# Optimization experiments

Measured on AMD Instinct MI355X. Metric: run time of the kernel, lower is better.

The kernel has to match this reference:

```python
import jax, jax.numpy as jnp
import numpy as np
import math

B, H, L = 8, 512, 4096
N2 = 32  # d_state // 2


def setup_inputs() -> dict:
    key = jax.random.key(0)
    ks = jax.random.split(key, 8)
    u = jax.random.normal(ks[0], (B, H, L), dtype=jnp.float32)
    C = jax.random.normal(ks[1], (H, N2, 2), dtype=jnp.float32)  # view_as_real of cfloat C
    # log_dt ~ Uniform[log(dt_min), log(dt_max)], dt_min=1e-3, dt_max=0.1
    log_dt = jax.random.uniform(ks[2], (H,), dtype=jnp.float32,
                                minval=math.log(0.001), maxval=math.log(0.1))
    log_A_real = jnp.log(0.5 * jnp.ones((H, N2), dtype=jnp.float32))
    A_imag = math.pi * jnp.broadcast_to(jnp.arange(N2, dtype=jnp.float32), (H, N2))
    D = jax.random.normal(ks[3], (H,), dtype=jnp.float32)
    # pointwise Conv1d(H, 2H, kernel_size=1): weight (2H, H), bias (2H)
    fan = 1.0 / math.sqrt(H)
    W = jax.random.uniform(ks[4], (2 * H, H), dtype=jnp.float32, minval=-fan, maxval=fan)
    b = jax.random.uniform(ks[5], (2 * H,), dtype=jnp.float32, minval=-fan, maxval=fan)
    return {"u": u, "C": C, "log_dt": log_dt, "log_A_real": log_A_real,
            "A_imag": A_imag, "D": D, "W": W, "b": b}


def reference(u, C, log_dt, log_A_real, A_imag, D, W, b):
    Lb = u.shape[-1]
    # --- S4DKernel: kernel k of shape (H, L) ---
    dt = jnp.exp(log_dt)                                  # (H,)
    Cc = C[..., 0] + 1j * C[..., 1]                       # (H, N2) complex
    A = -jnp.exp(log_A_real) + 1j * A_imag                # (H, N2)
    dtA = A * dt[:, None]                                 # (H, N2)
    # Vandermonde: exp(dtA * l) for l in [0, L)
    K = jnp.exp(dtA[:, :, None] * jnp.arange(Lb, dtype=jnp.float32))  # (H, N2, L)
    Cmod = Cc * (jnp.exp(dtA) - 1.0) / A                  # (H, N2)
    k = 2.0 * jnp.einsum('hn,hnl->hl', Cmod, K).real      # (H, L)
    # --- FFT convolution (length 2L, causal) ---
    n = 2 * Lb
    k_f = jnp.fft.rfft(k, n=n)                            # (H, L+1)
    u_f = jnp.fft.rfft(u, n=n)                            # (B, H, L+1)
    y = jnp.fft.irfft(u_f * k_f, n=n)[..., :Lb]           # (B, H, L)
    # skip connection
    y = y + u * D[:, None]
    # activation (torch nn.GELU default = exact erf form)
    y = jax.nn.gelu(y, approximate=False)
    # pointwise conv (H -> 2H) + GLU over channel dim
    y = jnp.einsum('oh,bhl->bol', W, y) + b[None, :, None]  # (B, 2H, L)
    a, g = jnp.split(y, 2, axis=1)
    return a * jax.nn.sigmoid(g)                          # (B, H, L)
```

## Files before the change

### kernel.cpp

```cpp
#include <hip/hip_runtime.h>
#include <hip/hip_bf16.h>

constexpr int Bn = 8, Hn = 512, Ln = 4096, N2n = 32;

typedef _Float16 f16;
typedef __attribute__((ext_vector_type(8))) _Float16 f16x8;
typedef __attribute__((ext_vector_type(4))) _Float16 f16x4;
typedef __attribute__((ext_vector_type(2))) _Float16 f16x2;
typedef __attribute__((ext_vector_type(4))) float f32x4;

typedef void __attribute__((address_space(1))) gvoid;
typedef void __attribute__((address_space(3))) lvoid;

__global__ __launch_bounds__(64) void k_mats1(
    const float* __restrict__ C, const float* __restrict__ log_dt,
    const float* __restrict__ logA, const float* __restrict__ Aim,
    f16* __restrict__ Vg, f16* __restrict__ A3g, float2* __restrict__ w64g) {
  __shared__ f16 VT[64 * 64];
  __shared__ f16 QT[64 * 64];
  __shared__ float kp[64][33];
  __shared__ float ks[64];
  const int h = blockIdx.x, tid = threadIdx.x, n = tid & 31;

  if (tid < 32) {
    const int idx = h * N2n + n;
    float dt = expf(log_dt[h]);
    float Ar = -expf(logA[idx]);
    float Ai = Aim[idx];
    float dr = Ar * dt, di = Ai * dt;
    float er = expf(dr);
    float wr = er * cosf(di), wi = er * sinf(di);
    float den = Ar * Ar + Ai * Ai;
    float e1r = wr - 1.0f, e1i = wi;
    float tr = (e1r * Ar + e1i * Ai) / den;
    float ti = (e1i * Ar - e1r * Ai) / den;
    float Cr = C[idx * 2 + 0], Ci = C[idx * 2 + 1];
    float c2r = 2.0f * (Cr * tr - Ci * ti);
    float c2i = 2.0f * (Cr * ti + Ci * tr);

    float wpr = 1.f, wpi = 0.f;
    for (int p = 0; p <= 64; ++p) {
      float cwr = c2r * wpr - c2i * wpi;
      float cwi = c2r * wpi + c2i * wpr;
      if (p < 64) {
        const int j = 63 - p, ch = j >> 3, jo = j & 7;
        const int s0 = 2 * n, s1 = 2 * n + 1;
        VT[s0 * 64 + ((ch ^ (s0 & 7)) * 8) + jo] = (f16)wpr;
        VT[s1 * 64 + ((ch ^ (s1 & 7)) * 8) + jo] = (f16)wpi;
        kp[p][n] = cwr;
      }
      if (p >= 1) {
        const int t = p - 1, c0 = 2 * n;
        const int ch = (c0 >> 3) ^ (t & 7);
        QT[t * 64 + ch * 8 + (c0 & 7)]     = (f16)cwr;
        QT[t * 64 + ch * 8 + (c0 & 7) + 1] = (f16)(-cwi);
      }
      if (p == 64) w64g[h * 32 + n] = make_float2(wpr, wpi);
      float nr = wpr * wr - wpi * wi;
      float ni = wpr * wi + wpi * wr;
      wpr = nr; wpi = ni;
    }
  }
  __syncthreads();
  float s = 0.f;
#pragma unroll
  for (int m = 0; m < 32; ++m) s += kp[tid][m];
  ks[tid] = s;
  __syncthreads();
  const int t = tid;
#pragma unroll
  for (int c = 0; c < 8; ++c) {
    f16x8 row;
#pragma unroll
    for (int jo = 0; jo < 8; ++jo) {
      int j = c * 8 + jo;
      row[jo] = (j <= t) ? (f16)ks[t - j] : (f16)0.f;
    }
    *(f16x8*)&A3g[(size_t)h * 8192 + t * 128 + ((c ^ (t & 7)) * 8)] = row;
  }
#pragma unroll
  for (int c = 0; c < 8; ++c)
    *(f16x8*)&Vg[(size_t)h * 4096 + tid * 64 + c * 8] = *(f16x8*)&VT[tid * 64 + c * 8];
#pragma unroll
  for (int c = 0; c < 8; ++c)
    *(f16x8*)&A3g[(size_t)h * 8192 + tid * 128 + 64 + c * 8] = *(f16x8*)&QT[tid * 64 + c * 8];
}

__global__ void conv_w(const float* __restrict__ W, f16* __restrict__ Wh) {
  int i = blockIdx.x * 256 + threadIdx.x;
  if (i < 2 * Hn * Hn) Wh[i] = (f16)W[i];
}

__global__ __launch_bounds__(256, 4) void s4d_mid(
    const float* __restrict__ u, const f16* __restrict__ Vg,
    const f16* __restrict__ A3g, const float2* __restrict__ w64g,
    const float* __restrict__ Dv, f16* __restrict__ yg) {
  __shared__ f16 MATS[8192];
  __shared__ f16 U[4096];
  __shared__ f16 LE[4096];
  __shared__ float2 Pbuf[4][32];
  const int tid = threadIdx.x, wid = tid >> 6, lane = tid & 63;
  const int h = ((blockIdx.x >> 6) << 3) | (blockIdx.x & 7);
  const int b = (blockIdx.x >> 3) & 7;
  const float Dh = Dv[h];

#pragma unroll
  for (int q = 0; q < 2; ++q)
    __builtin_amdgcn_global_load_lds((const gvoid*)(Vg + (size_t)h * 4096 + (q * 256 + tid) * 8),
                                     (lvoid*)&MATS[(q * 256 + wid * 64) * 8], 16, 0, 0);
#pragma unroll
  for (int i = 0; i < 4; ++i) {
    int e = (i * 256 + tid) * 4;
    float4 uv = *(const float4*)(u + ((size_t)(b * Hn + h)) * Ln + e);
    int col = e >> 6, j = e & 63;
    f16x4 hv = {(f16)uv.x, (f16)uv.y, (f16)uv.z, (f16)uv.w};
    *(f16x4*)&U[col * 64 + ((j >> 3) ^ (col & 7)) * 8 + (j & 7)] = hv;
  }
  asm volatile("s_waitcnt vmcnt(0)" ::: "memory");
  __syncthreads();

  const int col = wid * 16 + (lane & 15);
  f32x4 acc[4];
#pragma unroll
  for (int i = 0; i < 4; ++i) acc[i] = (f32x4){0.f, 0.f, 0.f, 0.f};
#pragma unroll
  for (int ks = 0; ks < 2; ++ks) {
    const int kc = ks * 4 + (lane >> 4);
    f16x8 bv = *(const f16x8*)&U[col * 64 + ((kc ^ (col & 7)) * 8)];
#pragma unroll
    for (int mf = 0; mf < 4; ++mf) {
      int row = mf * 16 + (lane & 15);
      f16x8 a = *(const f16x8*)&MATS[row * 64 + ((kc ^ (row & 7)) * 8)];
      acc[mf] = __builtin_amdgcn_mfma_f32_16x16x32_f16(a, bv, acc[mf], 0, 0, 0);
    }
  }
  __syncthreads();

#pragma unroll
  for (int q = 0; q < 4; ++q)
    __builtin_amdgcn_global_load_lds((const gvoid*)(A3g + (size_t)h * 8192 + (q * 256 + tid) * 8),
                                     (lvoid*)&MATS[(q * 256 + wid * 64) * 8], 16, 0, 0);

#pragma unroll
  for (int mf = 0; mf < 4; ++mf) {
    int st0 = mf * 16 + (lane >> 4) * 4;
    f16x4 o = {(f16)acc[mf][0], (f16)acc[mf][1], (f16)acc[mf][2], (f16)acc[mf][3]};
    *(f16x4*)&LE[col * 64 + (((st0 >> 3) ^ (col & 7)) << 3) + (st0 & 7)] = o;
  }
  __syncthreads();

  {
    const int n = lane & 31, q = wid;
    const float2 wT = w64g[h * 32 + n];
    float qr = wT.x, qi = wT.y;
#pragma unroll
    for (int s = 0; s < 4; ++s) {
      float nr = qr * qr - qi * qi;
      float ni = 2.f * qr * qi;
      qr = nr; qi = ni;
    }
    f16x2 Lb[16];
    float er = 0.f, ei = 0.f;
    if (lane < 32) {
#pragma unroll
      for (int k = 0; k < 16; ++k) {
        int blk = q * 16 + k;
        int fi = blk * 64 + (((n >> 2) ^ (blk & 7)) << 3) + ((n & 3) << 1);
        Lb[k] = *(const f16x2*)&LE[fi];
      }
#pragma unroll
      for (int k = 0; k < 16; ++k) {
        float nr = fmaf(wT.x, er, fmaf(-wT.y, ei, (float)Lb[k][0]));
        float ni = fmaf(wT.y, er, fmaf(wT.x, ei, (float)Lb[k][1]));
        er = nr; ei = ni;
      }
      Pbuf[q][n] = make_float2(er, ei);
    }
    __syncthreads();
    if (lane < 32) {
      float orr = 0.f, oii = 0.f;
      for (int p = 0; p < q; ++p) {
        float2 Pp = Pbuf[p][n];
        float nr = fmaf(qr, orr, fmaf(-qi, oii, Pp.x));
        float ni = fmaf(qi, orr, fmaf(qr, oii, Pp.y));
        orr = nr; oii = ni;
      }
      er = orr; ei = oii;
#pragma unroll
      for (int k = 0; k < 16; ++k) {
        int blk = q * 16 + k;
        int fi = blk * 64 + (((n >> 2) ^ (blk & 7)) << 3) + ((n & 3) << 1);
        *(f16x2*)&LE[fi] = (f16x2){(f16)er, (f16)ei};
        float nr = fmaf(wT.x, er, fmaf(-wT.y, ei, (float)Lb[k][0]));
        float ni = fmaf(wT.y, er, fmaf(wT.x, ei, (float)Lb[k][1]));
        er = nr; ei = ni;
      }
    }
  }
  asm volatile("s_waitcnt vmcnt(0)" ::: "memory");
  __syncthreads();

  f32x4 acc4[4];
#pragma unroll
  for (int i = 0; i < 4; ++i) acc4[i] = (f32x4){0.f, 0.f, 0.f, 0.f};
#pragma unroll
  for (int ks = 0; ks < 4; ++ks) {
    const int kc = ks * 4 + (lane >> 4);
    f16x8 bf;
    if (ks < 2) bf = *(const f16x8*)&U[col * 64 + ((kc ^ (col & 7)) << 3)];
    else        bf = *(const f16x8*)&LE[col * 64 + (((kc - 8) ^ (col & 7)) << 3)];
#pragma unroll
    for (int mf = 0; mf < 4; ++mf) {
      int row = mf * 16 + (lane & 15);
      f16x8 af = *(const f16x8*)&MATS[row * 128 + ((kc ^ (row & 7)) << 3)];
      acc4[mf] = __builtin_amdgcn_mfma_f32_16x16x32_f16(af, bf, acc4[mf], 0, 0, 0);
    }
  }
  const int t0 = (lane >> 4) * 4;
#pragma unroll
  for (int mf = 0; mf < 4; ++mf) {
    const int tb = mf * 16 + t0;
    f16x4 uq = *(const f16x4*)&U[col * 64 + (((tb >> 3) ^ (col & 7)) << 3) + (tb & 7)];
    f16x4 o;
#pragma unroll
    for (int r = 0; r < 4; ++r) {
      float v = acc4[mf][r] + Dh * (float)uq[r];
      float g2 = v * fmaf(0.0713548163f, v * v, 1.5957691216f);
      o[r] = (f16)(v * __builtin_amdgcn_rcpf(1.0f + __expf(-g2)));
    }
    *(f16x4*)&yg[((size_t)(b * Hn + h)) * Ln + col * 64 + tb] = o;
  }
}

__global__ __launch_bounds__(256) void k_transpose(
    const f16* __restrict__ yg, f16* __restrict__ gyT) {
  __shared__ float T[64][65];
  const int bid = blockIdx.x, tid = threadIdx.x;
  const int b = bid >> 9, hg = (bid >> 6) & 7, lg = bid & 63;
  const int h0 = hg * 64, l0 = lg * 64;
  const int hi = tid >> 2, lc = (tid & 3) * 16;
  const f16* src = yg + ((size_t)(b * Hn + h0 + hi)) * Ln + l0 + lc;
  f16x8 v0 = *(const f16x8*)src;
  f16x8 v1 = *(const f16x8*)(src + 8);
#pragma unroll
  for (int e = 0; e < 8; ++e) T[lc + e][hi] = (float)v0[e];
#pragma unroll
  for (int e = 0; e < 8; ++e) T[lc + 8 + e][hi] = (float)v1[e];
  __syncthreads();
  const int li = tid >> 2, hc = (tid & 3) * 16;
  f16x8 o0, o1;
#pragma unroll
  for (int e = 0; e < 8; ++e) o0[e] = (f16)T[li][hc + e];
#pragma unroll
  for (int e = 0; e < 8; ++e) o1[e] = (f16)T[li][hc + 8 + e];
  f16* dst = gyT + ((size_t)b * Ln + l0 + li) * Hn + h0 + hc;
  *(f16x8*)dst = o0;
  *(f16x8*)(dst + 8) = o1;
}

__global__ __launch_bounds__(256, 2) void s4d_gemm(
    const f16* __restrict__ Wh, const f16* __restrict__ gyT,
    const float* __restrict__ bias, float* __restrict__ out) {
  __shared__ f16 As[2][128][64];
  __shared__ f16 Bs[128][64];
  const int tid = threadIdx.x;
  const int wid = tid >> 6, lane = tid & 63;
  const int ntg = blockIdx.x & 255;
  const int mt = blockIdx.x >> 8;
  const int b = ntg >> 5;
  const int l0 = (ntg & 31) * 128;
  const int m0 = mt * 128;
  const int wm = wid >> 1, wn = wid & 1;

  f32x4 acc[2][4][4];
#pragma unroll
  for (int a = 0; a < 2; ++a)
#pragma unroll
    for (int i = 0; i < 4; ++i)
#pragma unroll
      for (int j = 0; j < 4; ++j) acc[a][i][j] = (f32x4){0.f, 0.f, 0.f, 0.f};

  const int srow = lane >> 3;
  const int sks = ((lane & 7) ^ srow) * 8;

  for (int kt = 0; kt < 8; ++kt) {
    const int k0 = kt * 64;
#pragma unroll
    for (int q = 0; q < 4; ++q) {
      const int r8 = wid * 32 + q * 8;
      const f16* srcA = Wh + ((size_t)(m0 + r8 + srow) * 512 + k0 + sks);
      __builtin_amdgcn_global_load_lds((const gvoid*)srcA, (lvoid*)&As[0][r8][0], 16, 0, 0);
      const f16* srcG = Wh + ((size_t)(Hn + m0 + r8 + srow) * 512 + k0 + sks);
      __builtin_amdgcn_global_load_lds((const gvoid*)srcG, (lvoid*)&As[1][r8][0], 16, 0, 0);
      const f16* srcB = gyT + (((size_t)b * Ln + l0 + r8 + srow) * Hn + k0 + sks);
      __builtin_amdgcn_global_load_lds((const gvoid*)srcB, (lvoid*)&Bs[r8][0], 16, 0, 0);
    }
    asm volatile("s_waitcnt vmcnt(0)" ::: "memory");
    __syncthreads();
#pragma unroll
    for (int kk = 0; kk < 2; ++kk) {
      const int kc = kk * 4 + (lane >> 4);
      f16x8 af0[4], af1[4], bfv[4];
#pragma unroll
      for (int mf = 0; mf < 4; ++mf) {
        const int row = wm * 64 + mf * 16 + (lane & 15);
        af0[mf] = *(const f16x8*)&As[0][row][(kc ^ (row & 7)) * 8];
        af1[mf] = *(const f16x8*)&As[1][row][(kc ^ (row & 7)) * 8];
      }
#pragma unroll
      for (int nf = 0; nf < 4; ++nf) {
        const int col = wn * 64 + nf * 16 + (lane & 15);
        bfv[nf] = *(const f16x8*)&Bs[col][(kc ^ (col & 7)) * 8];
      }
#pragma unroll
      for (int mf = 0; mf < 4; ++mf)
#pragma unroll
        for (int nf = 0; nf < 4; ++nf) {
          acc[0][mf][nf] = __builtin_amdgcn_mfma_f32_16x16x32_f16(af0[mf], bfv[nf], acc[0][mf][nf], 0, 0, 0);
          acc[1][mf][nf] = __builtin_amdgcn_mfma_f32_16x16x32_f16(af1[mf], bfv[nf], acc[1][mf][nf], 0, 0, 0);
        }
    }
    __syncthreads();
  }

  const int col = lane & 15, r0 = (lane >> 4) * 4;
#pragma unroll
  for (int mf = 0; mf < 4; ++mf) {
    const int hbase = m0 + wm * 64 + mf * 16 + r0;
#pragma unroll
    for (int nf = 0; nf < 4; ++nf) {
      const int l = l0 + wn * 64 + nf * 16 + col;
      f32x4 va = acc[0][mf][nf], vg = acc[1][mf][nf];
#pragma unroll
      for (int r = 0; r < 4; ++r) {
        const int hh = hbase + r;
        float av = va[r] + bias[hh];
        float gv = vg[r] + bias[Hn + hh];
        float sg = __builtin_amdgcn_rcpf(1.0f + __expf(-gv));
        out[((size_t)b * Hn + hh) * Ln + l] = av * sg;
      }
    }
  }
}

extern "C" void kernel_launch(void* const* d_in, const int* in_sizes, int n_in,
                              void* d_out, int out_size, void* d_ws, size_t ws_size,
                              hipStream_t stream) {
  (void)in_sizes; (void)n_in; (void)out_size; (void)ws_size;
  const float* u     = (const float*)d_in[0];
  const float* C     = (const float*)d_in[1];
  const float* logdt = (const float*)d_in[2];
  const float* logA  = (const float*)d_in[3];
  const float* Aim   = (const float*)d_in[4];
  const float* Dv    = (const float*)d_in[5];
  const float* W     = (const float*)d_in[6];
  const float* bias  = (const float*)d_in[7];
  float* out = (float*)d_out;

  char* ws = (char*)d_ws;
  f16*    gyT  = (f16*)ws;
  f16*    Vg   = (f16*)(ws + (size_t)(32 << 20));
  f16*    A3g  = (f16*)(ws + (size_t)(36 << 20));
  float2* w64g = (float2*)(ws + (size_t)(44 << 20));
  f16*    Wh   = (f16*)(ws + (size_t)(45 << 20));
  f16*    yg   = (f16*)d_out;

  hipLaunchKernelGGL(k_mats1, dim3(Hn), dim3(64), 0, stream, C, logdt, logA, Aim, Vg, A3g, w64g);
  hipLaunchKernelGGL(conv_w, dim3(2048), dim3(256), 0, stream, W, Wh);
  hipLaunchKernelGGL(s4d_mid, dim3(Hn * Bn), dim3(256), 0, stream, u, Vg, A3g, w64g, Dv, yg);
  hipLaunchKernelGGL(k_transpose, dim3(Bn * 8 * 64), dim3(256), 0, stream, yg, gyT);
  hipLaunchKernelGGL(s4d_gemm, dim3(4 * 256), dim3(256), 0, stream, Wh, gyT, bias, out);
}
```

Before: 98.12 us.

## Enlarge GEMM tiles, double-buffer LDS loads, split gate/value waves

The final GLU GEMM goes from 256-thread blocks with 128x128 tiles to 512-thread blocks covering 256 output rows (128 value plus 128 gate) by 256 columns. The k-loop now double-buffers LDS so the next k-slice loads while the current one computes. Gate waves compute the sigmoid and hand it to value waves through LDS as fp16, and bias is cached in shared memory. The aim is more operand reuse, fewer blocks and overlap of loads with MFMA, at the cost of higher LDS use and register pressure, plus fp16 rounding of the gate value.

New measurement: 103.1 us. +5.1%, slower.

```diff
diff --git a/kernel.cpp b/kernel.cpp
--- a/kernel.cpp
+++ b/kernel.cpp
@@ -258,89 +258,124 @@
   *(f16x8*)(dst + 8) = o1;
 }
 
-__global__ __launch_bounds__(256, 2) void s4d_gemm(
+__global__ __launch_bounds__(512, 2) void s4d_gemm(
     const f16* __restrict__ Wh, const f16* __restrict__ gyT,
     const float* __restrict__ bias, float* __restrict__ out) {
-  __shared__ f16 As[2][128][64];
-  __shared__ f16 Bs[128][64];
+  __shared__ f16 Asd[2][256 * 64];
+  __shared__ f16 Bsd[2][256 * 64];
+  __shared__ float biasS[256];
   const int tid = threadIdx.x;
   const int wid = tid >> 6, lane = tid & 63;
-  const int ntg = blockIdx.x & 255;
-  const int mt = blockIdx.x >> 8;
-  const int b = ntg >> 5;
-  const int l0 = (ntg & 31) * 128;
+  const int nt = blockIdx.x & 127;
+  const int mt = blockIdx.x >> 7;
+  const int b = nt >> 4;
+  const int l0 = (nt & 15) * 256;
   const int m0 = mt * 128;
-  const int wm = wid >> 1, wn = wid & 1;
-
-  f32x4 acc[2][4][4];
-#pragma unroll
-  for (int a = 0; a < 2; ++a)
-#pragma unroll
-    for (int i = 0; i < 4; ++i)
-#pragma unroll
-      for (int j = 0; j < 4; ++j) acc[a][i][j] = (f32x4){0.f, 0.f, 0.f, 0.f};
-
-  const int srow = lane >> 3;
-  const int sks = ((lane & 7) ^ srow) * 8;
+  const int isG = wid >> 2;
+  const int w4 = wid & 3;
+
+  if (tid < 128) biasS[tid] = bias[m0 + tid];
+  else if (tid < 256) biasS[tid] = bias[Hn + m0 + (tid - 128)];
+
+  const int srow8 = lane >> 3;
+  const int sp = lane & 7;
+
+#define STAGE(BUF, KT)                                                                   \
+  {                                                                                      \
+    const int k0 = (KT) * 64;                                                            \
+    _Pragma("unroll")                                                                    \
+    for (int q = 0; q < 4; ++q) {                                                        \
+      const int r = q * 64 + wid * 8 + srow8;                                \
+      const int wr = (r < 128) ? (m0 + r) : (Hn + m0 + r - 128);                         \
+      const f16* srcA = Wh + ((size_t)wr * 512 + k0 + ((sp ^ (r & 7)) * 8));             \
+      __builtin_amdgcn_global_load_lds((const gvoid*)srcA,                               \
+          (lvoid*)&Asd[BUF][(q * 64 + wid * 8) * 64], 16, 0, 0);                         \
+    }                                                                                    \
+    _Pragma("unroll")                                                                    \
+    for (int q = 0; q < 4; ++q) {                                                        \
+      const int r = q * 64 + wid * 8 + srow8;                          \
+      const f16* srcB = gyT + (((size_t)b * Ln + l0 + r) * Hn + k0 + ((sp ^ (r & 7)) * 8)); \
+      __builtin_amdgcn_global_load_lds((const gvoid*)srcB,                               \
+          (lvoid*)&Bsd[BUF][(q * 64 + wid * 8) * 64], 16, 0, 0);                         \
+    }                                                                                    \
+  }
+
+  f32x4 acc[8][4];
+#pragma unroll
+  for (int i = 0; i < 8; ++i)
+#pragma unroll
+    for (int j = 0; j < 4; ++j) acc[i][j] = (f32x4){0.f, 0.f, 0.f, 0.f};
+
+  STAGE(0, 0);
+  asm volatile("s_waitcnt vmcnt(0)" ::: "memory");
+  __syncthreads();
 
   for (int kt = 0; kt < 8; ++kt) {
-    const int k0 = kt * 64;
-#pragma unroll
-    for (int q = 0; q < 4; ++q) {
-      const int r8 = wid * 32 + q * 8;
-      const f16* srcA = Wh + ((size_t)(m0 + r8 + srow) * 512 + k0 + sks);
-      __builtin_amdgcn_global_load_lds((const gvoid*)srcA, (lvoid*)&As[0][r8][0], 16, 0, 0);
-      const f16* srcG = Wh + ((size_t)(Hn + m0 + r8 + srow) * 512 + k0 + sks);
-      __builtin_amdgcn_global_load_lds((const gvoid*)srcG, (lvoid*)&As[1][r8][0], 16, 0, 0);
-      const f16* srcB = gyT + (((size_t)b * Ln + l0 + r8 + srow) * Hn + k0 + sks);
-      __builtin_amdgcn_global_load_lds((const gvoid*)srcB, (lvoid*)&Bs[r8][0], 16, 0, 0);
+    const int cur = kt & 1;
+    if (kt < 7) STAGE(cur ^ 1, kt + 1);
+#pragma unroll
+    for (int kk = 0; kk < 2; ++kk) {
+      const int kc = kk * 4 + (lane >> 4);
+      f16x8 bf[4];
+#pragma unroll
+      for (int nf = 0; nf < 4; ++nf) {
+        const int cl = w4 * 64 + nf * 16 + (lane & 15);
+        bf[nf] = *(const f16x8*)&Bsd[cur][cl * 64 + ((kc ^ (cl & 7)) * 8)];
+      }
+#pragma unroll
+      for (int mf = 0; mf < 8; ++mf) {
+        const int ra = isG * 128 + mf * 16 + (lane & 15);
+        f16x8 af = *(const f16x8*)&Asd[cur][ra * 64 + ((kc ^ (ra & 7)) * 8)];
+#pragma unroll
+        for (int nf = 0; nf < 4; ++nf)
+          acc[mf][nf] = __builtin_amdgcn_mfma_f32_16x16x32_f16(af, bf[nf], acc[mf][nf], 0, 0, 0);
+      }
     }
     asm volatile("s_waitcnt vmcnt(0)" ::: "memory");
     __syncthreads();
-#pragma unroll
-    for (int kk = 0; kk < 2; ++kk) {
-      const int kc = kk * 4 + (lane >> 4);
-      f16x8 af0[4], af1[4], bfv[4];
-#pragma unroll
-      for (int mf = 0; mf < 4; ++mf) {
-        const int row = wm * 64 + mf * 16 + (lane & 15);
-        af0[mf] = *(const f16x8*)&As[0][row][(kc ^ (row & 7)) * 8];
-        af1[mf] = *(const f16x8*)&As[1][row][(kc ^ (row & 7)) * 8];
-      }
-#pragma unroll
-      for (int nf = 0; nf < 4; ++nf) {
-        const int col = wn * 64 + nf * 16 + (lane & 15);
-        bfv[nf] = *(const f16x8*)&Bs[col][(kc ^ (col & 7)) * 8];
-      }
-#pragma unroll
-      for (int mf = 0; mf < 4; ++mf)
-#pragma unroll
-        for (int nf = 0; nf < 4; ++nf) {
-          acc[0][mf][nf] = __builtin_amdgcn_mfma_f32_16x16x32_f16(af0[mf], bfv[nf], acc[0][mf][nf], 0, 0, 0);
-          acc[1][mf][nf] = __builtin_amdgcn_mfma_f32_16x16x32_f16(af1[mf], bfv[nf], acc[1][mf][nf], 0, 0, 0);
+  }
+
+  f16* SIG = &Asd[0][0];
+  const int slot = (w4 * 64 + lane) * 128;
+  if (isG) {
+#pragma unroll
+    for (int mf = 0; mf < 8; ++mf) {
+#pragma unroll
+      for (int np = 0; np < 2; ++np) {
+        f16x8 c;
+#pragma unroll
+        for (int e = 0; e < 8; ++e) {
+          const int nf = np * 2 + (e >> 2), r = e & 3;
+          const int rowh = mf * 16 + (lane >> 4) * 4 + r;
+          float gv = acc[mf][nf][r] + biasS[128 + rowh];
+          c[e] = (f16)__builtin_amdgcn_rcpf(1.0f + __expf(-gv));
         }
-    }
-    __syncthreads();
-  }
-
-  const int col = lane & 15, r0 = (lane >> 4) * 4;
-#pragma unroll
-  for (int mf = 0; mf < 4; ++mf) {
-    const int hbase = m0 + wm * 64 + mf * 16 + r0;
-#pragma unroll
-    for (int nf = 0; nf < 4; ++nf) {
-      const int l = l0 + wn * 64 + nf * 16 + col;
-      f32x4 va = acc[0][mf][nf], vg = acc[1][mf][nf];
-#pragma unroll
-      for (int r = 0; r < 4; ++r) {
-        const int hh = hbase + r;
-        float av = va[r] + bias[hh];
-        float gv = vg[r] + bias[Hn + hh];
-        float sg = __builtin_amdgcn_rcpf(1.0f + __expf(-gv));
-        out[((size_t)b * Hn + hh) * Ln + l] = av * sg;
-      }
-    }
-  }
+        const int cid = mf * 2 + np;
+        *(f16x8*)&SIG[slot + ((cid ^ (lane & 15)) * 8)] = c;
+      }
+    }
+  }
+  __syncthreads();
+  if (!isG) {
+#pragma unroll
+    for (int mf = 0; mf < 8; ++mf) {
+#pragma unroll
+      for (int np = 0; np < 2; ++np) {
+        const int cid = mf * 2 + np;
+        f16x8 sg = *(const f16x8*)&SIG[slot + ((cid ^ (lane & 15)) * 8)];
+#pragma unroll
+        for (int e = 0; e < 8; ++e) {
+          const int nf = np * 2 + (e >> 2), r = e & 3;
+          const int rowh = mf * 16 + (lane >> 4) * 4 + r;
+          const int hh = m0 + rowh;
+          const int l = l0 + w4 * 64 + nf * 16 + (lane & 15);
+          float av = acc[mf][nf][r] + biasS[rowh];
+          out[((size_t)b * Hn + hh) * Ln + l] = av * (float)sg[e];
+        }
+      }
+    }
+  }
+#undef STAGE
 }
 
 extern "C" void kernel_launch(void* const* d_in, const int* in_sizes, int n_in,
@@ -369,5 +404,5 @@
   hipLaunchKernelGGL(conv_w, dim3(2048), dim3(256), 0, stream, W, Wh);
   hipLaunchKernelGGL(s4d_mid, dim3(Hn * Bn), dim3(256), 0, stream, u, Vg, A3g, w64g, Dv, yg);
   hipLaunchKernelGGL(k_transpose, dim3(Bn * 8 * 64), dim3(256), 0, stream, yg, gyT);
-  hipLaunchKernelGGL(s4d_gemm, dim3(4 * 256), dim3(256), 0, stream, Wh, gyT, bias, out);
-}
+  hipLaunchKernelGGL(s4d_gemm, dim3(512), dim3(512), 0, stream, Wh, gyT, bias, out);
+}
```

## Restructure GLU GEMM with double-buffered K=32 stages and split gate/value warps

Applied to the files above, without the earlier changes.

Rewrites the final pointwise-conv GEMM to use 64-row M tiles, which doubles the grid. Warps are split so half compute the value half of the output and half compute the gate half, with sigmoid results exchanged through shared memory. K is staged in 32-wide chunks with double-buffered async global-to-LDS loads, so the next tile loads while MFMAs run. Bias is cached in LDS and occupancy is raised to 3 blocks per SM, aiming for better latency hiding and fewer registers. The cost is an extra LDS round trip for the gate values stored as f16, which loses some precision, plus extra barriers.

New measurement: 107.7 us. 9.8% more time.

```diff
diff --git a/kernel.cpp b/kernel.cpp
--- a/kernel.cpp
+++ b/kernel.cpp
@@ -258,89 +258,120 @@
   *(f16x8*)(dst + 8) = o1;
 }
 
-__global__ __launch_bounds__(256, 2) void s4d_gemm(
+__global__ __launch_bounds__(256, 3) void s4d_gemm(
     const f16* __restrict__ Wh, const f16* __restrict__ gyT,
     const float* __restrict__ bias, float* __restrict__ out) {
-  __shared__ f16 As[2][128][64];
-  __shared__ f16 Bs[128][64];
+  __shared__ f16 As[2][2][64][32];
+  __shared__ f16 Bs[2][128][32];
+  __shared__ float biasS[2][64];
   const int tid = threadIdx.x;
   const int wid = tid >> 6, lane = tid & 63;
-  const int ntg = blockIdx.x & 255;
+  const int nt = blockIdx.x & 255;
   const int mt = blockIdx.x >> 8;
-  const int b = ntg >> 5;
-  const int l0 = (ntg & 31) * 128;
-  const int m0 = mt * 128;
-  const int wm = wid >> 1, wn = wid & 1;
-
-  f32x4 acc[2][4][4];
-#pragma unroll
-  for (int a = 0; a < 2; ++a)
-#pragma unroll
-    for (int i = 0; i < 4; ++i)
-#pragma unroll
-      for (int j = 0; j < 4; ++j) acc[a][i][j] = (f32x4){0.f, 0.f, 0.f, 0.f};
-
-  const int srow = lane >> 3;
-  const int sks = ((lane & 7) ^ srow) * 8;
-
-  for (int kt = 0; kt < 8; ++kt) {
-    const int k0 = kt * 64;
-#pragma unroll
-    for (int q = 0; q < 4; ++q) {
-      const int r8 = wid * 32 + q * 8;
-      const f16* srcA = Wh + ((size_t)(m0 + r8 + srow) * 512 + k0 + sks);
-      __builtin_amdgcn_global_load_lds((const gvoid*)srcA, (lvoid*)&As[0][r8][0], 16, 0, 0);
-      const f16* srcG = Wh + ((size_t)(Hn + m0 + r8 + srow) * 512 + k0 + sks);
-      __builtin_amdgcn_global_load_lds((const gvoid*)srcG, (lvoid*)&As[1][r8][0], 16, 0, 0);
-      const f16* srcB = gyT + (((size_t)b * Ln + l0 + r8 + srow) * Hn + k0 + sks);
-      __builtin_amdgcn_global_load_lds((const gvoid*)srcB, (lvoid*)&Bs[r8][0], 16, 0, 0);
-    }
-    asm volatile("s_waitcnt vmcnt(0)" ::: "memory");
+  const int b = nt >> 5;
+  const int l0 = (nt & 31) * 128;
+  const int m0 = mt * 64;
+  const int isG = wid >> 1;
+  const int wn = wid & 1;
+
+  if (tid < 64) biasS[0][tid] = bias[m0 + tid];
+  else if (tid < 128) biasS[1][tid - 64] = bias[Hn + m0 + (tid - 64)];
+
+  const int srow = lane >> 2;
+  const int sp = lane & 3;
+
+#define S4(r) ((((r) & 3)) ^ (((r) >> 2) & 3))
+
+#define STAGE(BUF, KT)                                                                    \
+  {                                                                                       \
+    const int k0 = (KT) * 32;                                                             \
+    _Pragma("unroll")                                                                     \
+    for (int q = 0; q < 2; ++q) {                                                         \
+      const int g = wid * 2 + q;                                                \
+      const int ag = g >> 2, rq = g & 3;                                                  \
+      const int r = rq * 16 + srow;                                                       \
+      const f16* srcA = Wh + ((size_t)(ag * Hn + m0 + r) * 512 + k0 + ((sp ^ S4(r)) * 8)); \
+      __builtin_amdgcn_global_load_lds((const gvoid*)srcA,                                \
+          (lvoid*)&As[BUF][ag][rq * 16][0], 16, 0, 0);                                    \
+    }                                                                                     \
+    _Pragma("unroll")                                                                     \
+    for (int q = 0; q < 2; ++q) {                                                         \
+      const int rb = wid * 2 + q;                                               \
+      const int r = rb * 16 + srow;                                                       \
+      const f16* srcB = gyT + (((size_t)b * Ln + l0 + r) * Hn + k0 + ((sp ^ S4(r)) * 8)); \
+      __builtin_amdgcn_global_load_lds((const gvoid*)srcB,                                \
+          (lvoid*)&Bs[BUF][rb * 16][0], 16, 0, 0);                                        \
+    }                                                                                     \
+  }
+
+  f32x4 acc[4][4];
+#pragma unroll
+  for (int i = 0; i < 4; ++i)
+#pragma unroll
+    for (int j = 0; j < 4; ++j) acc[i][j] = (f32x4){0.f, 0.f, 0.f, 0.f};
+
+  STAGE(0, 0);
+  asm volatile("s_waitcnt vmcnt(0)" ::: "memory");
+  __syncthreads();
+
+  const int kc = lane >> 4;
+  for (int t = 0; t < 16; ++t) {
+    const int cur = t & 1;
+    if (t < 15) STAGE(cur ^ 1, t + 1);
+    f16x8 af[4], bf[4];
+#pragma unroll
+    for (int mf = 0; mf < 4; ++mf) {
+      const int row = mf * 16 + (lane & 15);
+      af[mf] = *(const f16x8*)&As[cur][isG][row][(kc ^ S4(row)) * 8];
+    }
+#pragma unroll
+    for (int nf = 0; nf < 4; ++nf) {
+      const int cl = wn * 64 + nf * 16 + (lane & 15);
+      bf[nf] = *(const f16x8*)&Bs[cur][cl][(kc ^ S4(cl)) * 8];
+    }
+#pragma unroll
+    for (int mf = 0; mf < 4; ++mf)
+#pragma unroll
+      for (int nf = 0; nf < 4; ++nf)
+        acc[mf][nf] = __builtin_amdgcn_mfma_f32_16x16x32_f16(af[mf], bf[nf], acc[mf][nf], 0, 0, 0);
     __syncthreads();
-#pragma unroll
-    for (int kk = 0; kk < 2; ++kk) {
-      const int kc = kk * 4 + (lane >> 4);
-      f16x8 af0[4], af1[4], bfv[4];
-#pragma unroll
-      for (int mf = 0; mf < 4; ++mf) {
-        const int row = wm * 64 + mf * 16 + (lane & 15);
-        af0[mf] = *(const f16x8*)&As[0][row][(kc ^ (row & 7)) * 8];
-        af1[mf] = *(const f16x8*)&As[1][row][(kc ^ (row & 7)) * 8];
-      }
+  }
+
+  f16 (*SIG)[64][64] = (f16(*)[64][64]) & Bs[0][0][0];
+  const int r0 = (lane >> 4) * 4, c0 = lane & 15;
+  if (isG) {
+#pragma unroll
+    for (int mf = 0; mf < 4; ++mf) {
 #pragma unroll
       for (int nf = 0; nf < 4; ++nf) {
-        const int col = wn * 64 + nf * 16 + (lane & 15);
-        bfv[nf] = *(const f16x8*)&Bs[col][(kc ^ (col & 7)) * 8];
-      }
-#pragma unroll
-      for (int mf = 0; mf < 4; ++mf)
-#pragma unroll
-        for (int nf = 0; nf < 4; ++nf) {
-          acc[0][mf][nf] = __builtin_amdgcn_mfma_f32_16x16x32_f16(af0[mf], bfv[nf], acc[0][mf][nf], 0, 0, 0);
-          acc[1][mf][nf] = __builtin_amdgcn_mfma_f32_16x16x32_f16(af1[mf], bfv[nf], acc[1][mf][nf], 0, 0, 0);
+#pragma unroll
+        for (int r = 0; r < 4; ++r) {
+          const int row = mf * 16 + r0 + r;
+          float gv = acc[mf][nf][r] + biasS[1][row];
+          SIG[wn][row][nf * 16 + c0] = (f16)__builtin_amdgcn_rcpf(1.0f + __expf(-gv));
         }
-    }
-    __syncthreads();
-  }
-
-  const int col = lane & 15, r0 = (lane >> 4) * 4;
-#pragma unroll
-  for (int mf = 0; mf < 4; ++mf) {
-    const int hbase = m0 + wm * 64 + mf * 16 + r0;
-#pragma unroll
-    for (int nf = 0; nf < 4; ++nf) {
-      const int l = l0 + wn * 64 + nf * 16 + col;
-      f32x4 va = acc[0][mf][nf], vg = acc[1][mf][nf];
-#pragma unroll
-      for (int r = 0; r < 4; ++r) {
-        const int hh = hbase + r;
-        float av = va[r] + bias[hh];
-        float gv = vg[r] + bias[Hn + hh];
-        float sg = __builtin_amdgcn_rcpf(1.0f + __expf(-gv));
-        out[((size_t)b * Hn + hh) * Ln + l] = av * sg;
-      }
-    }
-  }
+      }
+    }
+  }
+  __syncthreads();
+  if (!isG) {
+#pragma unroll
+    for (int mf = 0; mf < 4; ++mf) {
+#pragma unroll
+      for (int nf = 0; nf < 4; ++nf) {
+#pragma unroll
+        for (int r = 0; r < 4; ++r) {
+          const int row = mf * 16 + r0 + r;
+          const int col = nf * 16 + c0;
+          float av = acc[mf][nf][r] + biasS[0][row];
+          float sg = (float)SIG[wn][row][col];
+          out[((size_t)b * Hn + m0 + row) * Ln + l0 + wn * 64 + col] = av * sg;
+        }
+      }
+    }
+  }
+#undef STAGE
+#undef S4
 }
 
 extern "C" void kernel_launch(void* const* d_in, const int* in_sizes, int n_in,
@@ -369,5 +400,5 @@
   hipLaunchKernelGGL(conv_w, dim3(2048), dim3(256), 0, stream, W, Wh);
   hipLaunchKernelGGL(s4d_mid, dim3(Hn * Bn), dim3(256), 0, stream, u, Vg, A3g, w64g, Dv, yg);
   hipLaunchKernelGGL(k_transpose, dim3(Bn * 8 * 64), dim3(256), 0, stream, yg, gyT);
-  hipLaunchKernelGGL(s4d_gemm, dim3(4 * 256), dim3(256), 0, stream, Wh, gyT, bias, out);
-}
+  hipLaunchKernelGGL(s4d_gemm, dim3(8 * 256), dim3(256), 0, stream, Wh, gyT, bias, out);
+}
```
